# Kernel optimization log

Hardware: AMD Instinct MI355X
Metric: run time of the kernel (lower is better)

Reference implementation:

```python
import jax, jax.numpy as jnp
import numpy as np

LN2 = 0.6931471805599453

def ssp(t):
    # PhysNet shifted softplus
    return jax.nn.softplus(t) - LN2

N, F, K, E, NRES = 50000, 128, 64, 800000, 3

def setup_inputs() -> dict:
    key = jax.random.key(0)
    ks = jax.random.split(key, 16)
    d = {}
    d['x'] = jax.random.normal(ks[0], (N, F), dtype=jnp.float32)
    d['edge_index'] = jax.random.randint(ks[1], (2, E), 0, N, dtype=jnp.int64)
    d['edge_attr'] = jax.random.uniform(ks[2], (E, K), dtype=jnp.float32)
    s = 1.0 / np.sqrt(F)
    d['W_same'] = jax.random.normal(ks[3], (F, F), dtype=jnp.float32) * s
    d['b_same'] = jnp.zeros((F,), jnp.float32)
    d['W_diff'] = jax.random.normal(ks[4], (F, F), dtype=jnp.float32) * s
    d['b_diff'] = jnp.zeros((F,), jnp.float32)
    # G initialized to zero in the original; use small random so gradients flow
    d['W_G'] = jax.random.normal(ks[5], (F, K), dtype=jnp.float32) * 0.01
    d['res_W1'] = jax.random.normal(ks[6], (NRES, F, F), dtype=jnp.float32) * s
    d['res_b1'] = jnp.zeros((NRES, F), jnp.float32)
    d['res_W2'] = jax.random.normal(ks[7], (NRES, F, F), dtype=jnp.float32) * s
    d['res_b2'] = jnp.zeros((NRES, F), jnp.float32)
    d['W_last'] = jax.random.normal(ks[8], (F, F), dtype=jnp.float32) * s
    d['b_last'] = jnp.zeros((F,), jnp.float32)
    d['u'] = jnp.ones((1, F), jnp.float32)
    return d

def reference(x, edge_index, edge_attr, W_same, b_same, W_diff, b_diff, W_G,
              res_W1, res_b1, res_W2, res_b2, W_last, b_last, u):
    src, dst = edge_index[0], edge_index[1]  # flow='source_to_target': x_j = x[src], aggr at dst
    xa = ssp(x)                                           # activation(x) before propagate
    # message: act(lin_for_diff(x_j)) -- linear+act commute with gather, compute per-node
    h = ssp(xa @ W_diff.T + b_diff)                       # [N, F]
    gate = edge_attr @ W_G.T                              # [E, F]  G(edge_attr)
    msg = h[src] * gate                                   # [E, F]
    aggr = jax.ops.segment_sum(msg, dst, num_segments=x.shape[0])  # add-aggregate
    # update: act(lin_for_same(x)) + aggr_out
    msged_x = ssp(xa @ W_same.T + b_same) + aggr          # [N, F]
    # residual interaction layers: t + lin2(act(lin1(act(t))))
    t = msged_x
    for i in range(res_W1.shape[0]):
        h1 = ssp(ssp(t) @ res_W1[i].T + res_b1[i])
        t = t + (h1 @ res_W2[i].T + res_b2[i])
    v = ssp(t) @ W_last.T + b_last
    return (v + x * u, msged_x)
```

## Files before the change

kernel.cpp:

```cpp
#include <hip/hip_runtime.h>
#include <hip/hip_bf16.h>

#define LN2F 0.69314718055994530942f

typedef short bf16x8 __attribute__((ext_vector_type(8)));
typedef float f32x4  __attribute__((ext_vector_type(4)));

__device__ __forceinline__ float ssp_f(float t){
  return fmaxf(t, 0.0f) + __logf(1.0f + __expf(-fabsf(t))) - LN2F;
}
__device__ __forceinline__ unsigned short f2bf_u(float f){
  __hip_bfloat16 b = __float2bfloat16(f);
  return *reinterpret_cast<unsigned short*>(&b);
}
__device__ __forceinline__ float bf2f(unsigned short u){
  __hip_bfloat16 b = *reinterpret_cast<__hip_bfloat16*>(&u);
  return __bfloat162float(b);
}

__device__ __forceinline__ int load_idx(const void* ei, int is32, size_t pos){
  return is32 ? ((const int*)ei)[pos] : (int)(((const long long*)ei)[pos]);
}

struct WPtrs { const float* w[16]; };

__global__ __launch_bounds__(256) void setup_prep_kernel(
    const unsigned* __restrict__ ei, int* __restrict__ flag,
    int* __restrict__ count, int N, int nzb,
    WPtrs p, int nw, unsigned short* __restrict__ wfrag,
    const float* __restrict__ WG, unsigned short* __restrict__ wgfrag){
  const int m = blockIdx.x;
  if (m < nzb){
    int i = m * 256 + threadIdx.x;
    if (i < N) count[i] = 0;
    if (m == 0){
      __shared__ int cnt;
      if (threadIdx.x == 0) cnt = 0;
      __syncthreads();
      int nz = 0;
      for (int k = threadIdx.x; k < 1024; k += 256)
        nz += (ei[2*k + 1] != 0u) ? 1 : 0;
      atomicAdd(&cnt, nz);
      __syncthreads();
      if (threadIdx.x == 0) *flag = (cnt > 64) ? 1 : 0;
    }
  } else if (m < nzb + nw){
    const int w = m - nzb;
    const float* __restrict__ W = p.w[w];
    unsigned short* __restrict__ out = wfrag + (size_t)w * 16384;
    for (int q = threadIdx.x; q < 16384; q += 256){
      int i = q & 7, lane = (q >> 3) & 63, kt = (q >> 9) & 3, ct = q >> 11;
      int row = ct*16 + (lane & 15);
      int k   = kt*32 + (lane >> 4)*8 + i;
      out[q] = f2bf_u(W[row*128 + k]);
    }
  } else {
    const int b = m - nzb - nw;
    for (int qq = threadIdx.x; qq < 2048; qq += 256){
      int q = b*2048 + qq;
      int i = q & 7, lane = (q >> 3) & 63, kt = (q >> 9) & 1, nt = (q >> 10) & 3, half = q >> 12;
      int f = half*64 + nt*16 + (lane & 15);
      int k = kt*32 + (lane >> 4)*8 + i;
      wgfrag[q] = f2bf_u(WG[(size_t)f*64 + k]);
    }
  }
}

__global__ void hist_kernel(const void* __restrict__ ei, const int* __restrict__ flag,
                            int* __restrict__ count, int E){
  const int is32 = *flag;
  for (long long e = (long long)blockIdx.x * 256 + threadIdx.x; e < E;
       e += (long long)gridDim.x * 256){
    int d = load_idx(ei, is32, (size_t)((long long)E + e));
    atomicAdd(&count[d], 1);
  }
}

__global__ __launch_bounds__(256) void scan1_kernel(const int* __restrict__ count,
                                                    int* __restrict__ bsum, int N){
  __shared__ int red[256];
  const int t = threadIdx.x;
  int i0 = blockIdx.x * 2048 + t * 8;
  int s = 0;
  #pragma unroll
  for (int r = 0; r < 8; ++r){ int i = i0 + r; s += (i < N) ? count[i] : 0; }
  red[t] = s;
  __syncthreads();
  for (int off = 128; off > 0; off >>= 1){
    if (t < off) red[t] += red[t + off];
    __syncthreads();
  }
  if (t == 0) bsum[blockIdx.x] = red[0];
}

__global__ void scan2_kernel(int* __restrict__ bsum, int* __restrict__ offs, int nb, int N){
  if (threadIdx.x == 0 && blockIdx.x == 0){
    int run = 0;
    for (int b = 0; b < nb; ++b){ int v = bsum[b]; bsum[b] = run; run += v; }
    offs[N] = run;
  }
}

__global__ __launch_bounds__(256) void scan3_kernel(const int* __restrict__ count,
                                                    const int* __restrict__ bsum,
                                                    int* __restrict__ offs,
                                                    int* __restrict__ cur, int N){
  __shared__ int red[256];
  const int t = threadIdx.x;
  int i0 = blockIdx.x * 2048 + t * 8;
  int v[8];
  int s = 0;
  #pragma unroll
  for (int r = 0; r < 8; ++r){ int i = i0 + r; v[r] = (i < N) ? count[i] : 0; s += v[r]; }
  red[t] = s;
  __syncthreads();
  #pragma unroll
  for (int off = 1; off < 256; off <<= 1){
    int tv = (t >= off) ? red[t - off] : 0;
    __syncthreads();
    red[t] += tv;
    __syncthreads();
  }
  int run = red[t] - s + bsum[blockIdx.x];
  #pragma unroll
  for (int r = 0; r < 8; ++r){
    int i = i0 + r;
    if (i < N){ offs[i] = run; cur[i] = run; }
    run += v[r];
  }
}

__global__ void fill_kernel(const void* __restrict__ ei, const int* __restrict__ flag,
                            int* __restrict__ cur, int2* __restrict__ se, int E){
  const int is32 = *flag;
  for (long long e = (long long)blockIdx.x * 256 + threadIdx.x; e < E;
       e += (long long)gridDim.x * 256){
    int s = load_idx(ei, is32, (size_t)e);
    int d = load_idx(ei, is32, (size_t)((long long)E + e));
    int slot = atomicAdd(&cur[d], 1);
    se[slot] = make_int2((int)e, s);
  }
}

__device__ __forceinline__ void mfma_gemm128s(const unsigned short* __restrict__ A_s,
                                              const unsigned short* __restrict__ Bf,
                                              int rbase, int lane, f32x4 acc[8]){
  #pragma unroll
  for (int ct = 0; ct < 8; ++ct) acc[ct] = (f32x4){0.f, 0.f, 0.f, 0.f};
  const int r  = rbase + (lane & 15);
  const int kg = lane >> 4;
  const int sw = (r & 7) << 3;
  #pragma unroll
  for (int kt = 0; kt < 4; ++kt){
    bf16x8 a = *(const bf16x8*)&A_s[r*128 + ((kt*32 + kg*8) ^ sw)];
    #pragma unroll
    for (int ct = 0; ct < 8; ++ct){
      bf16x8 b = *(const bf16x8*)&Bf[(size_t)((ct*4 + kt)*64 + lane)*8];
      acc[ct] = __builtin_amdgcn_mfma_f32_16x16x32_bf16(a, b, acc[ct], 0, 0, 0);
    }
  }
}

__device__ __forceinline__ void stage_bf512(unsigned short* __restrict__ Bf,
                                            const unsigned short* __restrict__ src, int t){
  #pragma unroll
  for (int it = 0; it < 4; ++it){
    int off = (it*512 + t) * 8;
    *(uint4*)&Bf[off] = *(const uint4*)&src[off];
  }
}

__global__ __launch_bounds__(512) void node_dual_kernel(
    const float* __restrict__ x, const unsigned short* __restrict__ wfrag,
    const float* __restrict__ bsame, const float* __restrict__ bdiff,
    unsigned short* __restrict__ hbf, float* __restrict__ msged, int N){
  __shared__ __align__(16) unsigned short A_s[128*128];
  __shared__ __align__(16) unsigned short Bf[16384];
  const int t = threadIdx.x, wv = t >> 6, lane = t & 63;
  const int kg = lane >> 4, c = lane & 15;
  const int row0 = blockIdx.x * 128;
  for (int q = t; q < 2048; q += 512){
    int row = q >> 4, c0 = (q & 15) * 8;
    float4 va = make_float4(0.f,0.f,0.f,0.f), vb = va;
    if (row0 + row < N){
      va = *(const float4*)&x[(size_t)(row0 + row)*128 + c0];
      vb = *(const float4*)&x[(size_t)(row0 + row)*128 + c0 + 4];
    }
    uint4 w;
    w.x = f2bf_u(ssp_f(va.x)) | ((unsigned)f2bf_u(ssp_f(va.y)) << 16);
    w.y = f2bf_u(ssp_f(va.z)) | ((unsigned)f2bf_u(ssp_f(va.w)) << 16);
    w.z = f2bf_u(ssp_f(vb.x)) | ((unsigned)f2bf_u(ssp_f(vb.y)) << 16);
    w.w = f2bf_u(ssp_f(vb.z)) | ((unsigned)f2bf_u(ssp_f(vb.w)) << 16);
    *(uint4*)&A_s[row*128 + (c0 ^ ((row & 7) << 3))] = w;
  }
  stage_bf512(Bf, wfrag, t);
  __syncthreads();
  f32x4 acc[8];
  mfma_gemm128s(A_s, Bf, wv*16, lane, acc);
  #pragma unroll
  for (int ct = 0; ct < 8; ++ct){
    int col = ct*16 + c;
    float bv = bsame[col];
    #pragma unroll
    for (int q = 0; q < 4; ++q){
      int gr = row0 + wv*16 + kg*4 + q;
      if (gr < N) msged[(size_t)gr*128 + col] = ssp_f(acc[ct][q] + bv);
    }
  }
  __syncthreads();
  stage_bf512(Bf, wfrag + 16384, t);
  __syncthreads();
  mfma_gemm128s(A_s, Bf, wv*16, lane, acc);
  #pragma unroll
  for (int ct = 0; ct < 8; ++ct){
    int col = ct*16 + c;
    float bv = bdiff[col];
    #pragma unroll
    for (int q = 0; q < 4; ++q){
      int gr = row0 + wv*16 + kg*4 + q;
      if (gr < N) hbf[(size_t)gr*128 + col] = f2bf_u(ssp_f(acc[ct][q] + bv));
    }
  }
}

__global__ __launch_bounds__(256) void edge_mfma_kernel(
    const float* __restrict__ ea, const unsigned short* __restrict__ wgfrag,
    const unsigned short* __restrict__ h, const int2* __restrict__ se,
    const int* __restrict__ offs, float* __restrict__ msged, int N, int E, int KW){
  __shared__ float P_s[4][16][67];
  const int t = threadIdx.x, wv = t >> 6, lane = t & 63;
  const int kg = lane >> 4, c = lane & 15;
  const int gw = blockIdx.x * 4 + wv;
  const int half = gw & 1;
  const int widx = gw >> 1;
  if (widx >= KW) return;
  long long tt0 = (long long)widx * E / KW;
  long long tt1 = (long long)(widx + 1) * E / KW;
  int lo = 0, hi = N;
  while (lo < hi){ int mid = (lo + hi) >> 1; if ((long long)offs[mid] < tt0) lo = mid + 1; else hi = mid; }
  const int d_lo = lo;
  hi = N;
  while (lo < hi){ int mid = (lo + hi) >> 1; if ((long long)offs[mid] < tt1) lo = mid + 1; else hi = mid; }
  const int d_hi = lo;
  if (d_lo >= d_hi) return;
  const int s_beg = offs[d_lo], s_end = offs[d_hi];
  if (s_beg >= s_end) return;

  bf16x8 aw[4][2];
  #pragma unroll
  for (int nt = 0; nt < 4; ++nt)
    #pragma unroll
    for (int kt = 0; kt < 2; ++kt)
      aw[nt][kt] = *(const bf16x8*)&wgfrag[(size_t)((((half*4+nt)*2+kt)*64)+lane)*8];

  int d_cur = d_lo;
  int no0 = offs[d_cur + 1];
  while (no0 == s_beg && d_cur + 1 < d_hi){ ++d_cur; no0 = offs[d_cur + 1]; }
  int no1 = (d_cur + 2 <= d_hi) ? offs[d_cur + 2] : 0x7FFFFFFF;

  float sum_v = 0.f;
  int p = s_beg;
  int nb = min(16, s_end - p);
  int2 s2 = se[p + min(c, nb - 1)];
  while (p < s_end){
    const int pn = p + 16;
    int2 s2n = s2;
    if (pn < s_end){
      int nbn = min(16, s_end - pn);
      s2n = se[pn + min(c, nbn - 1)];
    }
    const float* __restrict__ ra = &ea[(size_t)s2.x * 64 + kg*8];
    float4 e00 = *(const float4*)&ra[0];
    float4 e01 = *(const float4*)&ra[4];
    float4 e10 = *(const float4*)&ra[32];
    float4 e11 = *(const float4*)&ra[36];
    const unsigned short* __restrict__ hr = &h[(size_t)s2.y*128 + half*64 + kg*4];
    ushort4 hu0 = *(const ushort4*)&hr[0];
    ushort4 hu1 = *(const ushort4*)&hr[16];
    ushort4 hu2 = *(const ushort4*)&hr[32];
    ushort4 hu3 = *(const ushort4*)&hr[48];

    bf16x8 be0, be1;
    unsigned short* b0p = (unsigned short*)&be0;
    unsigned short* b1p = (unsigned short*)&be1;
    b0p[0]=f2bf_u(e00.x); b0p[1]=f2bf_u(e00.y); b0p[2]=f2bf_u(e00.z); b0p[3]=f2bf_u(e00.w);
    b0p[4]=f2bf_u(e01.x); b0p[5]=f2bf_u(e01.y); b0p[6]=f2bf_u(e01.z); b0p[7]=f2bf_u(e01.w);
    b1p[0]=f2bf_u(e10.x); b1p[1]=f2bf_u(e10.y); b1p[2]=f2bf_u(e10.z); b1p[3]=f2bf_u(e10.w);
    b1p[4]=f2bf_u(e11.x); b1p[5]=f2bf_u(e11.y); b1p[6]=f2bf_u(e11.z); b1p[7]=f2bf_u(e11.w);

    f32x4 acc[4];
    #pragma unroll
    for (int nt = 0; nt < 4; ++nt){
      acc[nt] = (f32x4){0.f,0.f,0.f,0.f};
      acc[nt] = __builtin_amdgcn_mfma_f32_16x16x32_bf16(aw[nt][0], be0, acc[nt], 0, 0, 0);
      acc[nt] = __builtin_amdgcn_mfma_f32_16x16x32_bf16(aw[nt][1], be1, acc[nt], 0, 0, 0);
    }

    float hvv[4][4];
    hvv[0][0]=bf2f(hu0.x); hvv[0][1]=bf2f(hu0.y); hvv[0][2]=bf2f(hu0.z); hvv[0][3]=bf2f(hu0.w);
    hvv[1][0]=bf2f(hu1.x); hvv[1][1]=bf2f(hu1.y); hvv[1][2]=bf2f(hu1.z); hvv[1][3]=bf2f(hu1.w);
    hvv[2][0]=bf2f(hu2.x); hvv[2][1]=bf2f(hu2.y); hvv[2][2]=bf2f(hu2.z); hvv[2][3]=bf2f(hu2.w);
    hvv[3][0]=bf2f(hu3.x); hvv[3][1]=bf2f(hu3.y); hvv[3][2]=bf2f(hu3.z); hvv[3][3]=bf2f(hu3.w);

    #pragma unroll
    for (int nt = 0; nt < 4; ++nt)
      #pragma unroll
      for (int q = 0; q < 4; ++q)
        P_s[wv][c][nt*16 + kg*4 + q] = acc[nt][q] * hvv[nt][q];

    asm volatile("s_waitcnt lgkmcnt(0)" ::: "memory");

    float pv[16];
    #pragma unroll
    for (int i = 0; i < 16; ++i) pv[i] = P_s[wv][i][lane];

    const int nbc = min(16, s_end - p);
    #pragma unroll
    for (int i = 0; i < 16; ++i){
      if (i < nbc){
        sum_v += pv[i];
        if (p + i + 1 == no0){
          msged[(size_t)d_cur*128 + half*64 + lane] += sum_v;
          sum_v = 0.f;
          do {
            ++d_cur;
            no0 = no1;
            no1 = (d_cur + 2 <= d_hi) ? offs[d_cur + 2] : 0x7FFFFFFF;
          } while (no0 == p + i + 1);
        }
      }
    }
    p = pn; s2 = s2n;
  }
}

__global__ __launch_bounds__(512) void tail_kernel(
    const float* __restrict__ msged, const float* __restrict__ x, const float* __restrict__ u,
    const unsigned short* __restrict__ wfrag,
    const float* __restrict__ rb1, const float* __restrict__ rb2,
    const float* __restrict__ blast, float* __restrict__ out0, int N, int NRES){
  __shared__ __align__(16) unsigned short A_s[128*128];
  __shared__ __align__(16) unsigned short Bf[16384];
  const int t = threadIdx.x, wv = t >> 6, lane = t & 63;
  const int kg = lane >> 4, c = lane & 15;
  const int row0 = blockIdx.x * 128;

  float treg[8][4];
  #pragma unroll
  for (int ct = 0; ct < 8; ++ct)
    #pragma unroll
    for (int q = 0; q < 4; ++q){
      int gr = row0 + wv*16 + kg*4 + q;
      treg[ct][q] = (gr < N) ? msged[(size_t)gr*128 + ct*16 + c] : 0.f;
    }

  f32x4 acc[8];
  for (int l = 0; l < NRES; ++l){
    __syncthreads();
    #pragma unroll
    for (int ct = 0; ct < 8; ++ct)
      #pragma unroll
      for (int q = 0; q < 4; ++q){
        int row = wv*16 + kg*4 + q, col = ct*16 + c;
        A_s[row*128 + (col ^ ((row & 7) << 3))] = f2bf_u(ssp_f(treg[ct][q]));
      }
    stage_bf512(Bf, wfrag + (size_t)(2 + 2*l)*16384, t);
    __syncthreads();
    mfma_gemm128s(A_s, Bf, wv*16, lane, acc);
    __syncthreads();
    #pragma unroll
    for (int ct = 0; ct < 8; ++ct){
      float bv = rb1[l*128 + ct*16 + c];
      #pragma unroll
      for (int q = 0; q < 4; ++q){
        int row = wv*16 + kg*4 + q, col = ct*16 + c;
        A_s[row*128 + (col ^ ((row & 7) << 3))] = f2bf_u(ssp_f(acc[ct][q] + bv));
      }
    }
    stage_bf512(Bf, wfrag + (size_t)(3 + 2*l)*16384, t);
    __syncthreads();
    mfma_gemm128s(A_s, Bf, wv*16, lane, acc);
    #pragma unroll
    for (int ct = 0; ct < 8; ++ct){
      float bv = rb2[l*128 + ct*16 + c];
      #pragma unroll
      for (int q = 0; q < 4; ++q) treg[ct][q] += acc[ct][q] + bv;
    }
  }
  __syncthreads();
  #pragma unroll
  for (int ct = 0; ct < 8; ++ct)
    #pragma unroll
    for (int q = 0; q < 4; ++q){
      int row = wv*16 + kg*4 + q, col = ct*16 + c;
      A_s[row*128 + (col ^ ((row & 7) << 3))] = f2bf_u(ssp_f(treg[ct][q]));
    }
  stage_bf512(Bf, wfrag + (size_t)(2 + 2*NRES)*16384, t);
  __syncthreads();
  mfma_gemm128s(A_s, Bf, wv*16, lane, acc);
  #pragma unroll
  for (int ct = 0; ct < 8; ++ct){
    int col = ct*16 + c;
    float bv = blast[col];
    float uv = u[col];
    #pragma unroll
    for (int q = 0; q < 4; ++q){
      int gr = row0 + wv*16 + kg*4 + q;
      if (gr < N){
        size_t idx = (size_t)gr*128 + col;
        out0[idx] = acc[ct][q] + bv + x[idx]*uv;
      }
    }
  }
}

extern "C" void kernel_launch(void* const* d_in, const int* in_sizes, int n_in,
                              void* d_out, int out_size, void* d_ws, size_t ws_size,
                              hipStream_t stream){
  const float* x     = (const float*)d_in[0];
  const void*  ei    = d_in[1];
  const float* ea    = (const float*)d_in[2];
  const float* Wsame = (const float*)d_in[3];
  const float* bsame = (const float*)d_in[4];
  const float* Wdiff = (const float*)d_in[5];
  const float* bdiff = (const float*)d_in[6];
  const float* WG    = (const float*)d_in[7];
  const float* rW1   = (const float*)d_in[8];
  const float* rb1   = (const float*)d_in[9];
  const float* rW2   = (const float*)d_in[10];
  const float* rb2   = (const float*)d_in[11];
  const float* Wlast = (const float*)d_in[12];
  const float* blast = (const float*)d_in[13];
  const float* u     = (const float*)d_in[14];

  const int N    = in_sizes[0] / 128;
  const int E    = in_sizes[1] / 2;
  int NRES = in_sizes[8] / (128*128);
  if (NRES > 6) NRES = 6;

  float* out0  = (float*)d_out;
  float* msged = (float*)d_out + (size_t)N * 128;

  auto align256 = [](size_t v){ return (v + 255) & ~(size_t)255; };
  const size_t o_h      = 256;
  const size_t o_count  = align256(o_h      + (size_t)N * 128 * 2);
  const size_t o_off    = align256(o_count  + (size_t)N * 4);
  const size_t o_cur    = align256(o_off    + (size_t)(N + 1) * 4);
  const size_t o_se     = align256(o_cur    + (size_t)N * 4);
  const size_t o_bsum   = align256(o_se     + (size_t)E * 8);
  const size_t o_wfrag  = align256(o_bsum   + (size_t)4096 * 4);
  const size_t o_wgfrag = align256(o_wfrag  + (size_t)16 * 16384 * 2);

  int*   flag = (int*)d_ws;
  unsigned short* hbf = (unsigned short*)((char*)d_ws + o_h);
  int* count  = (int*)((char*)d_ws + o_count);
  int* offs   = (int*)((char*)d_ws + o_off);
  int* cur    = (int*)((char*)d_ws + o_cur);
  int2* se    = (int2*)((char*)d_ws + o_se);
  int* bsum   = (int*)((char*)d_ws + o_bsum);
  unsigned short* wfrag  = (unsigned short*)((char*)d_ws + o_wfrag);
  unsigned short* wgfrag = (unsigned short*)((char*)d_ws + o_wgfrag);
  (void)ws_size;

  const int nw = 3 + 2*NRES;
  WPtrs wp;
  wp.w[0] = Wsame;
  wp.w[1] = Wdiff;
  for (int l = 0; l < NRES; ++l){
    wp.w[2 + 2*l] = rW1 + (size_t)l*16384;
    wp.w[3 + 2*l] = rW2 + (size_t)l*16384;
  }
  wp.w[2 + 2*NRES] = Wlast;
  for (int i = nw; i < 16; ++i) wp.w[i] = Wlast;

  const int nb_node = (N + 127) / 128;
  const int nzb     = (N + 255) / 256;
  const int nbk     = (N + 2047) / 2048;
  const int nb_edge = 2048;
  const int KW = nb_edge * 4 / 2;

  setup_prep_kernel<<<nzb + nw + 4, 256, 0, stream>>>((const unsigned*)ei, flag, count, N,
                                                      nzb, wp, nw, wfrag, WG, wgfrag);
  node_dual_kernel<<<nb_node, 512, 0, stream>>>(x, wfrag, bsame, bdiff, hbf, msged, N);

  hist_kernel<<<1024, 256, 0, stream>>>(ei, flag, count, E);
  scan1_kernel<<<nbk, 256, 0, stream>>>(count, bsum, N);
  scan2_kernel<<<1, 64, 0, stream>>>(bsum, offs, nbk, N);
  scan3_kernel<<<nbk, 256, 0, stream>>>(count, bsum, offs, cur, N);
  fill_kernel<<<1024, 256, 0, stream>>>(ei, flag, cur, se, E);

  edge_mfma_kernel<<<nb_edge, 256, 0, stream>>>(ea, wgfrag, hbf, se, offs, msged, N, E, KW);

  tail_kernel<<<nb_node, 512, 0, stream>>>(msged, x, u, wfrag, rb1, rb2, blast,
                                           out0, N, NRES);
}
```

Baseline: 367.4 us.

## Process all 128 features per wave in edge kernel, staging gathered h rows in LDS

The edge kernel previously split the 128 output features across two waves, so each wave reloaded edge_attr and re-searched offsets for the same edge range. Now each wave covers all 128 features with eight MFMA tiles. The wave's 16 gathered h rows are loaded cooperatively as 16-byte loads and staged in shared memory, and the gate results are written to LDS and combined there. This halves the edge_attr reads and the segment bookkeeping per edge, and makes the h gathers coalesced. In exchange it uses more registers for the eight weight fragments and more LDS, and each wave does twice the serial accumulation work.

```diff
diff --git a/kernel.cpp b/kernel.cpp
--- a/kernel.cpp
+++ b/kernel.cpp
@@ -58,8 +58,8 @@
     const int b = m - nzb - nw;
     for (int qq = threadIdx.x; qq < 2048; qq += 256){
       int q = b*2048 + qq;
-      int i = q & 7, lane = (q >> 3) & 63, kt = (q >> 9) & 1, nt = (q >> 10) & 3, half = q >> 12;
-      int f = half*64 + nt*16 + (lane & 15);
+      int i = q & 7, lane = (q >> 3) & 63, kt = (q >> 9) & 1, nt = q >> 10;
+      int f = nt*16 + (lane & 15);
       int k = kt*32 + (lane >> 4)*8 + i;
       wgfrag[q] = f2bf_u(WG[(size_t)f*64 + k]);
     }
@@ -227,12 +227,11 @@
     const float* __restrict__ ea, const unsigned short* __restrict__ wgfrag,
     const unsigned short* __restrict__ h, const int2* __restrict__ se,
     const int* __restrict__ offs, float* __restrict__ msged, int N, int E, int KW){
-  __shared__ float P_s[4][16][67];
+  __shared__ float gate_s[4][16][132];
+  __shared__ unsigned short h_s[4][16][136];
   const int t = threadIdx.x, wv = t >> 6, lane = t & 63;
   const int kg = lane >> 4, c = lane & 15;
-  const int gw = blockIdx.x * 4 + wv;
-  const int half = gw & 1;
-  const int widx = gw >> 1;
+  const int widx = blockIdx.x * 4 + wv;
   if (widx >= KW) return;
   long long tt0 = (long long)widx * E / KW;
   long long tt1 = (long long)(widx + 1) * E / KW;
@@ -246,19 +245,19 @@
   const int s_beg = offs[d_lo], s_end = offs[d_hi];
   if (s_beg >= s_end) return;
 
-  bf16x8 aw[4][2];
-  #pragma unroll
-  for (int nt = 0; nt < 4; ++nt)
+  bf16x8 aw[8][2];
+  #pragma unroll
+  for (int nt = 0; nt < 8; ++nt)
     #pragma unroll
     for (int kt = 0; kt < 2; ++kt)
-      aw[nt][kt] = *(const bf16x8*)&wgfrag[(size_t)((((half*4+nt)*2+kt)*64)+lane)*8];
+      aw[nt][kt] = *(const bf16x8*)&wgfrag[(size_t)(((nt*2+kt)*64)+lane)*8];
 
   int d_cur = d_lo;
   int no0 = offs[d_cur + 1];
   while (no0 == s_beg && d_cur + 1 < d_hi){ ++d_cur; no0 = offs[d_cur + 1]; }
   int no1 = (d_cur + 2 <= d_hi) ? offs[d_cur + 2] : 0x7FFFFFFF;
 
-  float sum_v = 0.f;
+  float sum0 = 0.f, sum1 = 0.f;
   int p = s_beg;
   int nb = min(16, s_end - p);
   int2 s2 = se[p + min(c, nb - 1)];
@@ -274,11 +273,21 @@
     float4 e01 = *(const float4*)&ra[4];
     float4 e10 = *(const float4*)&ra[32];
     float4 e11 = *(const float4*)&ra[36];
-    const unsigned short* __restrict__ hr = &h[(size_t)s2.y*128 + half*64 + kg*4];
-    ushort4 hu0 = *(const ushort4*)&hr[0];
-    ushort4 hu1 = *(const ushort4*)&hr[16];
-    ushort4 hu2 = *(const ushort4*)&hr[32];
-    ushort4 hu3 = *(const ushort4*)&hr[48];
+
+    uint4 hreg[4];
+    #pragma unroll
+    for (int it = 0; it < 4; ++it){
+      int j = it*64 + lane;
+      int row = j >> 4, seg = j & 15;
+      int sr = __shfl(s2.y, row, 16);
+      hreg[it] = *(const uint4*)&h[(size_t)sr*128 + seg*8];
+    }
+    #pragma unroll
+    for (int it = 0; it < 4; ++it){
+      int j = it*64 + lane;
+      int row = j >> 4, seg = j & 15;
+      *(uint4*)&h_s[wv][row][seg*8] = hreg[it];
+    }
 
     bf16x8 be0, be1;
     unsigned short* b0p = (unsigned short*)&be0;
@@ -288,40 +297,31 @@
     b1p[0]=f2bf_u(e10.x); b1p[1]=f2bf_u(e10.y); b1p[2]=f2bf_u(e10.z); b1p[3]=f2bf_u(e10.w);
     b1p[4]=f2bf_u(e11.x); b1p[5]=f2bf_u(e11.y); b1p[6]=f2bf_u(e11.z); b1p[7]=f2bf_u(e11.w);
 
-    f32x4 acc[4];
-    #pragma unroll
-    for (int nt = 0; nt < 4; ++nt){
-      acc[nt] = (f32x4){0.f,0.f,0.f,0.f};
-      acc[nt] = __builtin_amdgcn_mfma_f32_16x16x32_bf16(aw[nt][0], be0, acc[nt], 0, 0, 0);
-      acc[nt] = __builtin_amdgcn_mfma_f32_16x16x32_bf16(aw[nt][1], be1, acc[nt], 0, 0, 0);
-    }
-
-    float hvv[4][4];
-    hvv[0][0]=bf2f(hu0.x); hvv[0][1]=bf2f(hu0.y); hvv[0][2]=bf2f(hu0.z); hvv[0][3]=bf2f(hu0.w);
-    hvv[1][0]=bf2f(hu1.x); hvv[1][1]=bf2f(hu1.y); hvv[1][2]=bf2f(hu1.z); hvv[1][3]=bf2f(hu1.w);
-    hvv[2][0]=bf2f(hu2.x); hvv[2][1]=bf2f(hu2.y); hvv[2][2]=bf2f(hu2.z); hvv[2][3]=bf2f(hu2.w);
-    hvv[3][0]=bf2f(hu3.x); hvv[3][1]=bf2f(hu3.y); hvv[3][2]=bf2f(hu3.z); hvv[3][3]=bf2f(hu3.w);
-
-    #pragma unroll
-    for (int nt = 0; nt < 4; ++nt)
-      #pragma unroll
-      for (int q = 0; q < 4; ++q)
-        P_s[wv][c][nt*16 + kg*4 + q] = acc[nt][q] * hvv[nt][q];
+    #pragma unroll
+    for (int nt = 0; nt < 8; ++nt){
+      f32x4 acc = (f32x4){0.f,0.f,0.f,0.f};
+      acc = __builtin_amdgcn_mfma_f32_16x16x32_bf16(aw[nt][0], be0, acc, 0, 0, 0);
+      acc = __builtin_amdgcn_mfma_f32_16x16x32_bf16(aw[nt][1], be1, acc, 0, 0, 0);
+      *(f32x4*)&gate_s[wv][c][nt*16 + kg*4] = acc;
+    }
 
     asm volatile("s_waitcnt lgkmcnt(0)" ::: "memory");
-
-    float pv[16];
-    #pragma unroll
-    for (int i = 0; i < 16; ++i) pv[i] = P_s[wv][i][lane];
 
     const int nbc = min(16, s_end - p);
     #pragma unroll
     for (int i = 0; i < 16; ++i){
       if (i < nbc){
-        sum_v += pv[i];
+        float g0 = gate_s[wv][i][lane];
+        float g1 = gate_s[wv][i][lane + 64];
+        float h0 = bf2f(h_s[wv][i][lane]);
+        float h1 = bf2f(h_s[wv][i][lane + 64]);
+        sum0 = __builtin_fmaf(g0, h0, sum0);
+        sum1 = __builtin_fmaf(g1, h1, sum1);
         if (p + i + 1 == no0){
-          msged[(size_t)d_cur*128 + half*64 + lane] += sum_v;
-          sum_v = 0.f;
+          float* mp = &msged[(size_t)d_cur*128 + lane];
+          mp[0]  += sum0;
+          mp[64] += sum1;
+          sum0 = 0.f; sum1 = 0.f;
           do {
             ++d_cur;
             no0 = no1;
@@ -477,7 +477,7 @@
   const int nzb     = (N + 255) / 256;
   const int nbk     = (N + 2047) / 2048;
   const int nb_edge = 2048;
-  const int KW = nb_edge * 4 / 2;
+  const int KW = nb_edge * 4;
 
   setup_prep_kernel<<<nzb + nw + 4, 256, 0, stream>>>((const unsigned*)ei, flag, count, N,
                                                       nzb, wp, nw, wfrag, WG, wgfrag);
```

Result: no change. 360.7 us (-1.8%).
